# Kernel optimization log

Hardware: AMD Instinct MI355X
Metric: run time of the kernel (lower is better)

The kernel has to match this reference:

```python
import jax, jax.numpy as jnp
import numpy as np
from jax import lax

B, CODELEN, COMLEN, NAST, SUBG = 32, 50, 30, 300, 4
EMB, H, ASTHOPS = 300, 256, 2
AST_VOCAB, COM_VOCAB = 10000, 10000


def gru(x, h0, wih, whh, bih, bhh):
    # PyTorch GRU cell semantics. x: [N, T, D], h0: [N, H] -> (ys [N,T,H], hT [N,H])
    xg = jnp.einsum('ntd,gd->ntg', x, wih) + bih  # precompute input gates [N,T,3H]
    def step(h, xt):
        hg = h @ whh.T + bhh
        xr, xz, xn = jnp.split(xt, 3, axis=-1)
        hr, hz, hn = jnp.split(hg, 3, axis=-1)
        r = jax.nn.sigmoid(xr + hr)
        z = jax.nn.sigmoid(xz + hz)
        n = jnp.tanh(xn + r * hn)
        hnew = (1.0 - z) * n + z * h
        return hnew, hnew
    hT, ys = lax.scan(step, h0, jnp.swapaxes(xg, 0, 1))
    return jnp.swapaxes(ys, 0, 1), hT


def dot_attn(q, k):
    # DotProductAttention in eval mode (dropout = identity)
    scale = 1.0 / jnp.sqrt(jnp.asarray(q.shape[-1], q.dtype))
    s = jnp.einsum('bqd,bkd->bqk', q, k) * scale
    return jnp.einsum('bqk,bkd->bqd', jax.nn.softmax(s, axis=-1), k)


def setup_inputs() -> dict:
    key = jax.random.key(0)
    ks = jax.random.split(key, 32)
    def rn(k, shp, sc=0.05):
        return jax.random.normal(k, shp, jnp.float32) * sc
    inp = {}
    inp['x0'] = jax.random.randint(ks[0], (B, CODELEN), 0, AST_VOCAB)
    inp['x1'] = jax.random.randint(ks[1], (B, COMLEN), 0, COM_VOCAB)
    inp['x2'] = jax.random.randint(ks[2], (B, SUBG, NAST), 0, AST_VOCAB)
    inp['adj'] = jax.random.uniform(ks[3], (B, SUBG, NAST, NAST), jnp.float32) * (1.0 / NAST)
    inp['emb_ast'] = rn(ks[4], (AST_VOCAB, EMB), 0.5)
    inp['emb_com'] = rn(ks[5], (COM_VOCAB, EMB), 0.5)
    inp['gru1_wih'] = rn(ks[6], (3 * H, EMB)); inp['gru1_whh'] = rn(ks[7], (3 * H, H))
    inp['gru1_bih'] = rn(ks[8], (3 * H,));    inp['gru1_bhh'] = rn(ks[9], (3 * H,))
    inp['gru2_wih'] = rn(ks[10], (3 * H, EMB)); inp['gru2_whh'] = rn(ks[11], (3 * H, H))
    inp['gru2_bih'] = rn(ks[12], (3 * H,));     inp['gru2_bhh'] = rn(ks[13], (3 * H,))
    inp['gru4_wih'] = rn(ks[14], (3 * H, NAST * EMB), 0.01)
    inp['gru4_whh'] = rn(ks[15], (3 * H, H))
    inp['gru4_bih'] = rn(ks[16], (3 * H,)); inp['gru4_bhh'] = rn(ks[17], (3 * H,))
    inp['gru58_wih'] = rn(ks[18], (SUBG, 3 * H, EMB)); inp['gru58_whh'] = rn(ks[19], (SUBG, 3 * H, H))
    inp['gru58_bih'] = rn(ks[20], (SUBG, 3 * H));      inp['gru58_bhh'] = rn(ks[21], (SUBG, 3 * H))
    inp['gcn_w'] = rn(ks[22], (EMB, EMB)); inp['gcn_b'] = rn(ks[23], (EMB,))
    inp['dense_w'] = rn(ks[24], (H, 3 * H)); inp['dense_b'] = rn(ks[25], (H,))
    inp['lin_w'] = rn(ks[26], (COM_VOCAB, COMLEN * H), 0.01); inp['lin_b'] = rn(ks[27], (COM_VOCAB,))
    return inp


def reference(x0, x1, x2, adj, emb_ast, emb_com,
              gru1_wih, gru1_whh, gru1_bih, gru1_bhh,
              gru2_wih, gru2_whh, gru2_bih, gru2_bhh,
              gru4_wih, gru4_whh, gru4_bih, gru4_bhh,
              gru58_wih, gru58_whh, gru58_bih, gru58_bhh,
              gcn_w, gcn_b, dense_w, dense_b, lin_w, lin_b):
    b = x0.shape[0]
    scale = 1.0 / jnp.sqrt(jnp.float32(H))
    # token encoder + comment decoder
    tencout, tstate = gru(emb_ast[x0], jnp.zeros((b, H), jnp.float32),
                          gru1_wih, gru1_whh, gru1_bih, gru1_bhh)
    decout, _ = gru(emb_com[x1], tstate, gru2_wih, gru2_whh, gru2_bih, gru2_bhh)
    tcontext = dot_attn(decout, tencout)
    # GCN over 4 sub-graphs (torch code mutates astwork in place -> tmp alias sees post-GCN feats)
    astwork = jnp.transpose(emb_ast[x2], (1, 0, 2, 3))  # [4,B,N,300]
    adjp = jnp.transpose(adj, (1, 0, 2, 3))             # [4,B,N,N]
    for _ in range(ASTHOPS):
        support = jnp.einsum('sbnd,de->sbne', astwork, gcn_w)
        astwork = jax.nn.relu(jnp.einsum('sbnm,sbme->sbne', adjp, support) + gcn_b)
    # TimeDistributed(gru4): batch = 4 sub-graphs, sequence = B, input = flattened node feats
    g4in = astwork.reshape(SUBG, b, NAST * EMB)
    g4out, _ = gru(g4in, jnp.zeros((SUBG, H), jnp.float32),
                   gru4_wih, gru4_whh, gru4_bih, gru4_bhh)
    astw = jnp.transpose(g4out, (1, 0, 2))  # [B,4,H]
    ahier = jax.nn.softmax(jnp.einsum('bqd,bsd->bqs', decout, astw) * scale, axis=-1)
    ahier_p = jnp.transpose(ahier, (2, 0, 1))  # [4,B,Q]
    # per-sub-graph node GRUs (gru5..gru8) vmapped over the sub-graph axis
    outs, _ = jax.vmap(gru, in_axes=(0, None, 0, 0, 0, 0))(
        astwork, tstate, gru58_wih, gru58_whh, gru58_bih, gru58_bhh)  # [4,B,N,H]
    sc = jax.nn.softmax(jnp.einsum('bqd,sbkd->sbqk', decout, outs) * scale, axis=-1)
    new_atten = sc * ahier_p[:, :, :, None]  # element_wise_mul with hierarchy weights
    acontext = jnp.einsum('sbqk,sbkd->bqd', new_atten, outs)  # bmm then sum over sub-graphs
    acontext = dot_attn(decout, acontext)
    context = jnp.concatenate([tcontext, decout, acontext], axis=-1)  # [B,Q,768]
    out = jax.nn.relu(context @ dense_w.T + dense_b)
    out = out.reshape(b, -1)  # [B, 7680]
    return out @ lin_w.T + lin_b  # [B, comvocab]
```

## Files before the change

### kernel.cpp

```cpp
#include <hip/hip_runtime.h>
#include <hip/hip_fp16.h>
#include <hip/hip_bf16.h>


typedef __attribute__((ext_vector_type(8))) short  bf16x8;
typedef __attribute__((ext_vector_type(4))) float  f32x4;

__device__ inline unsigned short f2bs(float f) {
  __hip_bfloat16 h = __float2bfloat16(f);
  unsigned short u; __builtin_memcpy(&u, &h, 2); return u;
}
__device__ inline float bs2f(unsigned short u) {
  unsigned v = (unsigned)u << 16;
  float f; __builtin_memcpy(&f, &v, 4); return f;
}
__device__ inline float sigf(float x) { return 1.f / (1.f + __expf(-x)); }
__device__ inline float tanhf_(float x) {
  const float e = __expf(-2.f * fabsf(x));
  return copysignf((1.f - e) / (1.f + e), x);
}

template <bool ABF, bool BBF, int OUTM, bool RELU, bool GATHER = false, bool BKN = false>
__global__ __launch_bounds__(256) void k_mfma(
    const void* __restrict__ Av, long lda, long a_ss, long a_sb,
    const void* __restrict__ Bv, long ldb, long b_ss, long b_sb,
    void* __restrict__ Cv, long ldc, long c_ss, long c_sb,
    const float* __restrict__ bias, long bias_ss,
    const int* __restrict__ gidx,
    int M, int N, int K, int zb, int ksplit)
{
  __shared__ unsigned short As[128][40];
  __shared__ unsigned short Bs[128][40];
  const int tid = threadIdx.x;
  const int zi = blockIdx.z;
  const int bi = zi / ksplit;
  const int ks = zi - bi * ksplit;
  const int sIdx = bi / zb;
  const int bIdx = bi - sIdx * zb;
  const int row0 = blockIdx.y * 128;
  const int col0 = blockIdx.x * 128;
  const int Kc = ((K + ksplit * 32 - 1) / (ksplit * 32)) * 32;
  const int kbeg = ks * Kc;
  const int kend = min(K, kbeg + Kc);
  if (kbeg >= kend) return;

  const char* Ab = (const char*)Av + ((long)sIdx * a_ss + (long)bIdx * a_sb) * (ABF ? 2 : 4);
  const char* Bb = (const char*)Bv + ((long)sIdx * b_ss + (long)bIdx * b_sb) * (BBF ? 2 : 4);
  char* Cb = (char*)Cv + ((long)sIdx * c_ss + (long)bIdx * c_sb) * ((OUTM == 1 || OUTM == 3) ? 2 : 4);

  const int w = tid >> 6, l = tid & 63;
  const int wr = w >> 1, wc = w & 1;
  const int lr = l & 15, lg = l >> 4;

  f32x4 acc[4][4];
#pragma unroll
  for (int m = 0; m < 4; ++m)
#pragma unroll
    for (int n = 0; n < 4; ++n) acc[m][n] = f32x4{0.f, 0.f, 0.f, 0.f};

  const int sr = tid >> 1;
  const int sk = (tid & 1) * 16;

  for (int kt = kbeg; kt < kend; kt += 32) {
    {
      const int gr = row0 + sr;
      if (ABF) {
        const unsigned short* src = (const unsigned short*)(Ab + ((long)gr * lda + kt + sk) * 2);
        if (gr < M && kt + sk + 16 <= kend) {
          const uint2* p = (const uint2*)src;
          *(uint2*)&As[sr][sk + 0]  = p[0];
          *(uint2*)&As[sr][sk + 4]  = p[1];
          *(uint2*)&As[sr][sk + 8]  = p[2];
          *(uint2*)&As[sr][sk + 12] = p[3];
        } else {
#pragma unroll
          for (int i = 0; i < 16; ++i) {
            const int kk = kt + sk + i;
            As[sr][sk + i] = (gr < M && kk < kend) ? src[i] : (unsigned short)0;
          }
        }
      } else {
        const float* src;
        if (GATHER) src = (const float*)Av + ((gr < M) ? (long)gidx[gr] * lda : 0) + kt + sk;
        else        src = (const float*)(Ab + ((long)gr * lda + kt + sk) * 4);
        if (gr < M && kt + sk + 16 <= kend) {
#pragma unroll
          for (int q = 0; q < 4; ++q) {
            const float4 v = ((const float4*)src)[q];
            *(unsigned*)&As[sr][sk + q * 4 + 0] = (unsigned)f2bs(v.x) | ((unsigned)f2bs(v.y) << 16);
            *(unsigned*)&As[sr][sk + q * 4 + 2] = (unsigned)f2bs(v.z) | ((unsigned)f2bs(v.w) << 16);
          }
        } else {
#pragma unroll
          for (int i = 0; i < 16; ++i) {
            const int kk = kt + sk + i;
            As[sr][sk + i] = (gr < M && kk < kend) ? f2bs(src[i]) : (unsigned short)0;
          }
        }
      }
    }
    if (BKN) {
      const int kk = tid >> 3;
      const int cb = (tid & 7) * 16;
      const int gk = kt + kk;
#pragma unroll
      for (int q = 0; q < 16; ++q) {
        const int gc = col0 + cb + q;
        unsigned short v = 0;
        if (gk < kend && gc < N) {
          if (BBF) v = ((const unsigned short*)Bb)[(long)gk * ldb + gc];
          else     v = f2bs(((const float*)Bb)[(long)gk * ldb + gc]);
        }
        Bs[cb + q][kk] = v;
      }
    } else {
      const int gc = col0 + sr;
      if (BBF) {
        const unsigned short* src = (const unsigned short*)(Bb + ((long)gc * ldb + kt + sk) * 2);
        if (gc < N && kt + sk + 16 <= kend) {
          const uint2* p = (const uint2*)src;
          *(uint2*)&Bs[sr][sk + 0]  = p[0];
          *(uint2*)&Bs[sr][sk + 4]  = p[1];
          *(uint2*)&Bs[sr][sk + 8]  = p[2];
          *(uint2*)&Bs[sr][sk + 12] = p[3];
        } else {
#pragma unroll
          for (int i = 0; i < 16; ++i) {
            const int kk = kt + sk + i;
            Bs[sr][sk + i] = (gc < N && kk < kend) ? src[i] : (unsigned short)0;
          }
        }
      } else {
        const float* src = (const float*)(Bb + ((long)gc * ldb + kt + sk) * 4);
        if (gc < N && kt + sk + 16 <= kend) {
#pragma unroll
          for (int q = 0; q < 4; ++q) {
            const float4 v = ((const float4*)src)[q];
            *(unsigned*)&Bs[sr][sk + q * 4 + 0] = (unsigned)f2bs(v.x) | ((unsigned)f2bs(v.y) << 16);
            *(unsigned*)&Bs[sr][sk + q * 4 + 2] = (unsigned)f2bs(v.z) | ((unsigned)f2bs(v.w) << 16);
          }
        } else {
#pragma unroll
          for (int i = 0; i < 16; ++i) {
            const int kk = kt + sk + i;
            Bs[sr][sk + i] = (gc < N && kk < kend) ? f2bs(src[i]) : (unsigned short)0;
          }
        }
      }
    }
    __syncthreads();
    bf16x8 af[4], bf[4];
#pragma unroll
    for (int m = 0; m < 4; ++m)
      af[m] = *(const bf16x8*)&As[wr * 64 + m * 16 + lr][lg * 8];
#pragma unroll
    for (int n = 0; n < 4; ++n)
      bf[n] = *(const bf16x8*)&Bs[wc * 64 + n * 16 + lr][lg * 8];
#pragma unroll
    for (int m = 0; m < 4; ++m)
#pragma unroll
      for (int n = 0; n < 4; ++n)
        acc[m][n] = __builtin_amdgcn_mfma_f32_16x16x32_bf16(af[m], bf[n], acc[m][n], 0, 0, 0);
    __syncthreads();
  }

  const float* bp = bias ? bias + (long)sIdx * bias_ss : nullptr;
#pragma unroll
  for (int m = 0; m < 4; ++m) {
#pragma unroll
    for (int n = 0; n < 4; ++n) {
      const int col = col0 + wc * 64 + n * 16 + lr;
      const int rb  = row0 + wr * 64 + m * 16 + lg * 4;
      const f32x4 v = acc[m][n];
      if (col >= N) continue;
      if (OUTM == 3) {
        unsigned short* ct = (unsigned short*)Cb + (long)col * ldc + rb;
        if (rb + 4 <= M) {
          ushort4 pk;
          pk.x = f2bs(v[0]); pk.y = f2bs(v[1]); pk.z = f2bs(v[2]); pk.w = f2bs(v[3]);
          *(ushort4*)ct = pk;
        } else {
#pragma unroll
          for (int r = 0; r < 4; ++r) if (rb + r < M) ct[r] = f2bs(v[r]);
        }
      } else {
        const float bv = bp ? bp[col] : 0.f;
#pragma unroll
        for (int r = 0; r < 4; ++r) {
          const int row = rb + r;
          if (row >= M) continue;
          float x = v[r] + bv;
          if (RELU) x = fmaxf(x, 0.f);
          if (OUTM == 0) ((float*)Cb)[(long)row * ldc + col] = x;
          else if (OUTM == 1) ((unsigned short*)Cb)[(long)row * ldc + col] = f2bs(x);
          else atomicAdd((float*)Cb + (long)row * ldc + col, x);
        }
      }
    }
  }
}

template <int CPB, bool XBF, bool YBF>
__global__ __launch_bounds__(512, 2)
void k_gru_v5(
    const void* __restrict__ xg,
    const float* __restrict__ h0, int h0_mod,
    const unsigned short* __restrict__ whh_bf, long w_stride, int cpw,
    const float* __restrict__ bhh, long b_stride,
    void* __restrict__ ys, float* __restrict__ hT, int T)
{
  constexpr int ESZ  = XBF ? 2 : 4;
  constexpr int VPR  = 768 * ESZ / 16;
  constexpr int XVEC = CPB * VPR;
  constexpr int NQ   = (XVEC + 511) / 512;

  const int tid = threadIdx.x;
  const int c0  = blockIdx.x * CPB;
  const int wv  = tid >> 6;
  const int l   = tid & 63;
  const int lr  = l & 15;
  const int lg  = l >> 4;

  __shared__ unsigned short A_lds[2][8][64][8];
  __shared__ unsigned short w_lds[8][8][64][8];
  __shared__ float gate_lds[CPB][772];
  __shared__ float bhh_lds[768];
  __shared__ uint4 xbuf[2][XVEC];

  { unsigned* az = (unsigned*)A_lds;
    for (int i = tid; i < 4096; i += 512) az[i] = 0; }

  const unsigned short* W = whh_bf + (long)(c0 / cpw) * w_stride;
  bf16x8 bfr[5][8];
#pragma unroll
  for (int nt = 0; nt < 5; ++nt) {
    const unsigned short* wp = W + (long)(wv * 96 + nt * 16 + lr) * 256 + lg * 8;
#pragma unroll
    for (int kt = 0; kt < 8; ++kt) bfr[nt][kt] = *(const bf16x8*)(wp + kt * 32);
  }
  {
    const unsigned short* wp = W + (long)(wv * 96 + 5 * 16 + lr) * 256 + lg * 8;
#pragma unroll
    for (int kt = 0; kt < 8; ++kt)
      *(bf16x8*)&w_lds[wv][kt][l][0] = *(const bf16x8*)(wp + kt * 32);
  }
  for (int i = tid; i < 768; i += 512)
    bhh_lds[i] = bhh[(long)(c0 / cpw) * b_stride + i];
  __syncthreads();

  const int c   = tid >> 5;
  const int jb  = tid & 31;
  const bool act = c < CPB;
  const int u0  = jb * 8;

  float h[8];
  if (act) {
#pragma unroll
    for (int e = 0; e < 8; ++e)
      h[e] = h0 ? h0[(long)((c0 + c) % h0_mod) * 256 + u0 + e] : 0.f;
    bf16x8 pk;
#pragma unroll
    for (int e = 0; e < 8; ++e) pk[e] = (short)f2bs(h[e]);
    *(bf16x8*)&A_lds[0][jb >> 2][(jb & 3) * 16 + c][0] = pk;
  }

  const char* xbase = (const char*)xg + (long)c0 * T * 768 * ESZ;
  int poff[NQ]; bool pact[NQ];
#pragma unroll
  for (int q = 0; q < NQ; ++q) {
    const int i = tid + q * 512;
    pact[q] = i < XVEC;
    const int ci = pact[q] ? i / VPR : 0;
    const int of = i - ci * VPR;
    poff[q] = ci * T * 768 * ESZ + of * 16;
  }
#pragma unroll
  for (int q = 0; q < NQ; ++q)
    if (pact[q]) ((uint4*)xbuf[0])[tid + q * 512] = *(const uint4*)(xbase + poff[q]);
  __syncthreads();

  int cur = 0;
  for (int t = 0; t < T; ++t) {
    uint4 xs[NQ];
    const bool pf = (t + 1 < T);
    if (pf) {
#pragma unroll
      for (int q = 0; q < NQ; ++q)
        if (pact[q]) xs[q] = *(const uint4*)(xbase + poff[q] + (long)(t + 1) * 768 * ESZ);
    }

    f32x4 acc[6];
#pragma unroll
    for (int nt = 0; nt < 6; ++nt) acc[nt] = f32x4{0.f, 0.f, 0.f, 0.f};
#pragma unroll
    for (int kt = 0; kt < 8; ++kt) {
      const bf16x8 af = *(const bf16x8*)&A_lds[cur][kt][l][0];
#pragma unroll
      for (int nt = 0; nt < 5; ++nt)
        acc[nt] = __builtin_amdgcn_mfma_f32_16x16x32_bf16(af, bfr[nt][kt], acc[nt], 0, 0, 0);
      const bf16x8 wf = *(const bf16x8*)&w_lds[wv][kt][l][0];
      acc[5] = __builtin_amdgcn_mfma_f32_16x16x32_bf16(af, wf, acc[5], 0, 0, 0);
    }
    if (lg * 4 < CPB) {
#pragma unroll
      for (int nt = 0; nt < 6; ++nt) {
        const int col = wv * 96 + nt * 16 + lr;
#pragma unroll
        for (int r = 0; r < 4; ++r) gate_lds[lg * 4 + r][col] = acc[nt][r];
      }
    }
    __syncthreads();

    if (pf) {
#pragma unroll
      for (int q = 0; q < NQ; ++q)
        if (pact[q]) ((uint4*)xbuf[cur ^ 1])[tid + q * 512] = xs[q];
    }

    if (act) {
      float xr[8], xz[8], xn[8];
      if (XBF) {
        const unsigned short* xp = (const unsigned short*)xbuf[cur] + c * 768;
        const bf16x8 vr = *(const bf16x8*)(xp + u0);
        const bf16x8 vz = *(const bf16x8*)(xp + 256 + u0);
        const bf16x8 vn = *(const bf16x8*)(xp + 512 + u0);
#pragma unroll
        for (int e = 0; e < 8; ++e) {
          xr[e] = bs2f((unsigned short)vr[e]);
          xz[e] = bs2f((unsigned short)vz[e]);
          xn[e] = bs2f((unsigned short)vn[e]);
        }
      } else {
        const float* xp = (const float*)xbuf[cur] + c * 768;
        *(float4*)&xr[0] = *(const float4*)(xp + u0);
        *(float4*)&xr[4] = *(const float4*)(xp + u0 + 4);
        *(float4*)&xz[0] = *(const float4*)(xp + 256 + u0);
        *(float4*)&xz[4] = *(const float4*)(xp + 256 + u0 + 4);
        *(float4*)&xn[0] = *(const float4*)(xp + 512 + u0);
        *(float4*)&xn[4] = *(const float4*)(xp + 512 + u0 + 4);
      }
      bf16x8 pk;
#pragma unroll
      for (int e = 0; e < 8; ++e) {
        const int u = u0 + e;
        const float rr = sigf(xr[e] + gate_lds[c][u] + bhh_lds[u]);
        const float zz = sigf(xz[e] + gate_lds[c][256 + u] + bhh_lds[256 + u]);
        const float nv = tanhf_(xn[e] + rr * (gate_lds[c][512 + u] + bhh_lds[512 + u]));
        h[e] = (1.f - zz) * nv + zz * h[e];
        pk[e] = (short)f2bs(h[e]);
      }
      *(bf16x8*)&A_lds[cur ^ 1][jb >> 2][(jb & 3) * 16 + c][0] = pk;
      if (ys) {
        if (YBF) {
          *(bf16x8*)((unsigned short*)ys + ((long)(c0 + c) * T + t) * 256 + u0) = pk;
        } else {
          float* yp = (float*)ys + ((long)(c0 + c) * T + t) * 256 + u0;
          *(float4*)yp = float4{h[0], h[1], h[2], h[3]};
          *(float4*)(yp + 4) = float4{h[4], h[5], h[6], h[7]};
        }
      }
    }
    __syncthreads();
    cur ^= 1;
  }
  if (hT && act) {
    float* hp = hT + (long)(c0 + c) * 256 + u0;
    *(float4*)hp = float4{h[0], h[1], h[2], h[3]};
    *(float4*)(hp + 4) = float4{h[4], h[5], h[6], h[7]};
  }
}

__global__ __launch_bounds__(256) void k_init_bias(
    float* __restrict__ C, const float* __restrict__ bias, int M, int N)
{
  const int total = M * N;
  for (int i = blockIdx.x * 256 + threadIdx.x; i < total; i += gridDim.x * 256)
    C[i] = bias[i % N];
}

__global__ __launch_bounds__(256) void k_gather_ast(
    const float* __restrict__ emb, const int* __restrict__ x2,
    unsigned short* __restrict__ outp)
{
  const int total = 4 * 32 * 300 * 300;
  for (int idx = blockIdx.x * 256 + threadIdx.x; idx < total; idx += gridDim.x * 256) {
    const int d = idx % 300;
    const int r = idx / 300;
    const int n = r % 300;
    const int r2 = r / 300;
    const int b = r2 % 32;
    const int s = r2 / 32;
    outp[idx] = f2bs(emb[(long)x2[(b * 4 + s) * 300 + n] * 300 + d]);
  }
}

__global__ __launch_bounds__(256) void k_twb(
    const float* __restrict__ w, unsigned short* __restrict__ o, int R, int C)
{
  const int total = R * C;
  for (int i = blockIdx.x * 256 + threadIdx.x; i < total; i += gridDim.x * 256) {
    const int r = i / C, c = i - r * C;
    o[(long)c * R + r] = f2bs(w[i]);
  }
}

__global__ __launch_bounds__(256) void k_f2b(
    const float* __restrict__ a, unsigned short* __restrict__ o, int n)
{
  for (int i = blockIdx.x * 256 + threadIdx.x; i < n; i += gridDim.x * 256)
    o[i] = f2bs(a[i]);
}

__global__ __launch_bounds__(256) void k_attn(
    const float* __restrict__ q, const float* __restrict__ kv,
    float* __restrict__ out, int Q, int L)
{
  const int bq = blockIdx.x;
  const int b = bq / Q;
  const int tid = threadIdx.x;
  const int g = tid >> 3, l = tid & 7;
  __shared__ float qv[256];
  __shared__ float sc[64];
  qv[tid] = q[(long)bq * 256 + tid];
  __syncthreads();
  for (int k0 = 0; k0 < L; k0 += 32) {
    const int k = k0 + g;
    float s = 0.f;
    if (k < L) {
      const float* kr = kv + ((long)b * L + k) * 256;
      for (int d = l; d < 256; d += 8) s += qv[d] * kr[d];
    }
    s += __shfl_xor(s, 1);
    s += __shfl_xor(s, 2);
    s += __shfl_xor(s, 4);
    if (k < L && l == 0) sc[k] = s * 0.0625f;
  }
  __syncthreads();
  float m = -1e30f;
  for (int k = 0; k < L; ++k) m = fmaxf(m, sc[k]);
  float den = 0.f;
  for (int k = 0; k < L; ++k) den += __expf(sc[k] - m);
  __syncthreads();
  if (tid < L) sc[tid] = __expf(sc[tid] - m);
  __syncthreads();
  const float* kb = kv + (long)b * L * 256;
  float acc = 0.f;
  for (int k = 0; k < L; ++k) acc += sc[k] * kb[(long)k * 256 + tid];
  out[(long)bq * 256 + tid] = acc / den;
}

__global__ __launch_bounds__(64) void k_hier(
    const float* __restrict__ dec, const float* __restrict__ g4out,
    float* __restrict__ ahier, int Q)
{
  const int bq = blockIdx.x;
  const int b = bq / Q;
  const int l = threadIdx.x;
  float s[4] = {0.f, 0.f, 0.f, 0.f};
#pragma unroll
  for (int i = 0; i < 4; ++i) {
    const int d = l * 4 + i;
    const float qd = dec[(long)bq * 256 + d];
#pragma unroll
    for (int sg = 0; sg < 4; ++sg)
      s[sg] += qd * g4out[((long)sg * 32 + b) * 256 + d];
  }
#pragma unroll
  for (int off = 32; off >= 1; off >>= 1)
#pragma unroll
    for (int sg = 0; sg < 4; ++sg) s[sg] += __shfl_xor(s[sg], off);
  if (l == 0) {
    float m = -1e30f;
#pragma unroll
    for (int sg = 0; sg < 4; ++sg) m = fmaxf(m, s[sg] * 0.0625f);
    float e[4], den = 0.f;
#pragma unroll
    for (int sg = 0; sg < 4; ++sg) { e[sg] = __expf(s[sg] * 0.0625f - m); den += e[sg]; }
#pragma unroll
    for (int sg = 0; sg < 4; ++sg) ahier[(long)bq * 4 + sg] = e[sg] / den;
  }
}

__global__ __launch_bounds__(64) void k_smax(
    float* __restrict__ sc, const float* __restrict__ ahier)
{
  const int id = blockIdx.x;
  const int s = id / 960;
  const int bq = id - s * 960;
  float* row = sc + (long)id * 300;
  const int l = threadIdx.x;
  float v[5];
  float m = -1e30f;
#pragma unroll
  for (int i = 0; i < 5; ++i) {
    const int k = l + i * 64;
    v[i] = (k < 300) ? row[k] * 0.0625f : -1e30f;
    m = fmaxf(m, v[i]);
  }
#pragma unroll
  for (int off = 32; off >= 1; off >>= 1) m = fmaxf(m, __shfl_xor(m, off));
  float den = 0.f;
#pragma unroll
  for (int i = 0; i < 5; ++i) { v[i] = __expf(v[i] - m); den += v[i]; }
#pragma unroll
  for (int off = 32; off >= 1; off >>= 1) den += __shfl_xor(den, off);
  const float w = ahier[(long)bq * 4 + s] / den;
#pragma unroll
  for (int i = 0; i < 5; ++i) {
    const int k = l + i * 64;
    if (k < 300) row[k] = v[i] * w;
  }
}

__global__ __launch_bounds__(256) void k_concat(
    const float* __restrict__ a, const float* __restrict__ b,
    const float* __restrict__ c, float* __restrict__ out, int rows)
{
  const int total = rows * 768;
  for (int i = blockIdx.x * 256 + threadIdx.x; i < total; i += gridDim.x * 256) {
    const int r = i / 768, col = i - r * 768;
    float v;
    if (col < 256) v = a[(long)r * 256 + col];
    else if (col < 512) v = b[(long)r * 256 + col - 256];
    else v = c[(long)r * 256 + col - 512];
    out[i] = v;
  }
}

extern "C" void kernel_launch(void* const* d_in, const int* in_sizes, int n_in,
                              void* d_out, int out_size, void* d_ws, size_t ws_size,
                              hipStream_t stream) {
  const int*   x0      = (const int*)d_in[0];
  const int*   x1      = (const int*)d_in[1];
  const int*   x2      = (const int*)d_in[2];
  const float* adj     = (const float*)d_in[3];
  const float* emb_ast = (const float*)d_in[4];
  const float* emb_com = (const float*)d_in[5];
  const float* g1_wih  = (const float*)d_in[6];
  const float* g1_whh  = (const float*)d_in[7];
  const float* g1_bih  = (const float*)d_in[8];
  const float* g1_bhh  = (const float*)d_in[9];
  const float* g2_wih  = (const float*)d_in[10];
  const float* g2_whh  = (const float*)d_in[11];
  const float* g2_bih  = (const float*)d_in[12];
  const float* g2_bhh  = (const float*)d_in[13];
  const float* g4_wih  = (const float*)d_in[14];
  const float* g4_whh  = (const float*)d_in[15];
  const float* g4_bih  = (const float*)d_in[16];
  const float* g4_bhh  = (const float*)d_in[17];
  const float* g58_wih = (const float*)d_in[18];
  const float* g58_whh = (const float*)d_in[19];
  const float* g58_bih = (const float*)d_in[20];
  const float* g58_bhh = (const float*)d_in[21];
  const float* gcn_w   = (const float*)d_in[22];
  const float* gcn_b   = (const float*)d_in[23];
  const float* dw      = (const float*)d_in[24];
  const float* db      = (const float*)d_in[25];
  const float* lw      = (const float*)d_in[26];
  const float* lb      = (const float*)d_in[27];
  float* out = (float*)d_out;
  float* ws  = (float*)d_ws;

  unsigned short* astwork_bf = (unsigned short*)ws;
  unsigned short* supportT   = (unsigned short*)(ws + 5760000L);
  unsigned short* g58xg_bf   = (unsigned short*)(ws + 11520000L);
  unsigned short* outsb_bf   = (unsigned short*)(ws + 26265600L);
  unsigned short* xg1_bf     = (unsigned short*)(ws + 31180800L);
  unsigned short* xg2_bf     = (unsigned short*)(ws + 31795200L);
  float* tenc    = ws + 32163840L;
  float* tstate  = ws + 32573440L;
  float* dec     = ws + 32581632L;
  float* tctx    = ws + 32827392L;
  float* g4xg    = ws + 33073152L;
  float* g4out   = ws + 33171456L;
  float* ahier   = ws + 33204224L;
  float* actx1   = ws + 33208064L;
  float* actx    = ws + 33453824L;
  float* dense   = ws + 33699584L;
  float* ctmp    = ws + 33945344L;
  float* scbuf   = ws + 34682624L;
  unsigned short* gcn_wT    = (unsigned short*)(ws + 35834624L);
  unsigned short* dense_bf  = (unsigned short*)(ws + 35879624L);
  unsigned short* g1whh_bf  = (unsigned short*)(ws + 36002504L);
  unsigned short* g2whh_bf  = (unsigned short*)(ws + 36100808L);
  unsigned short* g4whh_bf  = (unsigned short*)(ws + 36199112L);
  unsigned short* g58whh_bf = (unsigned short*)(ws + 36297416L);
  unsigned short* adj_bf    = (unsigned short*)(ws + 36690632L);

  const dim3 blk(256);

  k_gather_ast<<<dim3(4096), blk, 0, stream>>>(emb_ast, x2, astwork_bf);
  k_twb<<<dim3(90), blk, 0, stream>>>(gcn_w, gcn_wT, 300, 300);
  k_f2b<<<dim3(192), blk, 0, stream>>>(g1_whh, g1whh_bf, 196608);
  k_f2b<<<dim3(192), blk, 0, stream>>>(g2_whh, g2whh_bf, 196608);
  k_f2b<<<dim3(192), blk, 0, stream>>>(g4_whh, g4whh_bf, 196608);
  k_f2b<<<dim3(768), blk, 0, stream>>>(g58_whh, g58whh_bf, 786432);
  k_f2b<<<dim3(4096), blk, 0, stream>>>(adj, adj_bf, 11520000);

  for (int hop = 0; hop < 2; ++hop) {
    k_mfma<true, true, 3, false><<<dim3(3, 3, 128), blk, 0, stream>>>(
        astwork_bf, 300, 2880000, 90000,
        gcn_wT, 300, 0, 0,
        supportT, 300, 2880000, 90000,
        nullptr, 0, nullptr, 300, 300, 300, 32, 1);
    k_mfma<true, true, 1, true><<<dim3(3, 3, 128), blk, 0, stream>>>(
        adj_bf, 300, 90000, 360000,
        supportT, 300, 2880000, 90000,
        astwork_bf, 300, 2880000, 90000,
        gcn_b, 0, nullptr, 300, 300, 300, 32, 1);
  }

  k_mfma<false, false, 1, false, true><<<dim3(6, 13, 1), blk, 0, stream>>>(
      emb_ast, 300, 0, 0, g1_wih, 300, 0, 0, xg1_bf, 768, 0, 0,
      g1_bih, 0, x0, 1600, 768, 300, 1, 1);
  k_gru_v5<8, true, false><<<dim3(4), dim3(512), 0, stream>>>(
      xg1_bf, nullptr, 1, g1whh_bf, 0, 32, g1_bhh, 0, tenc, tstate, 50);

  k_mfma<false, false, 1, false, true><<<dim3(6, 8, 1), blk, 0, stream>>>(
      emb_com, 300, 0, 0, g2_wih, 300, 0, 0, xg2_bf, 768, 0, 0,
      g2_bih, 0, x1, 960, 768, 300, 1, 1);
  k_gru_v5<8, true, false><<<dim3(4), dim3(512), 0, stream>>>(
      xg2_bf, tstate, 32, g2whh_bf, 0, 32, g2_bhh, 0, dec, nullptr, 30);

  k_attn<<<dim3(960), blk, 0, stream>>>(dec, tenc, tctx, 30, 50);

  k_init_bias<<<dim3(384), blk, 0, stream>>>(g4xg, g4_bih, 128, 768);
  k_mfma<true, false, 2, false><<<dim3(6, 1, 43), blk, 0, stream>>>(
      astwork_bf, 90000, 0, 0, g4_wih, 90000, 0, 0, g4xg, 768, 0, 0,
      nullptr, 0, nullptr, 128, 768, 90000, 1, 43);
  k_gru_v5<4, false, false><<<dim3(1), dim3(512), 0, stream>>>(
      g4xg, nullptr, 1, g4whh_bf, 0, 4, g4_bhh, 0, g4out, nullptr, 32);

  k_hier<<<dim3(960), dim3(64), 0, stream>>>(dec, g4out, ahier, 30);

  k_mfma<true, false, 1, false><<<dim3(6, 75, 4), blk, 0, stream>>>(
      astwork_bf, 300, 2880000, 0, g58_wih, 300, 230400, 0,
      g58xg_bf, 768, 7372800, 0, g58_bih, 768, nullptr, 9600, 768, 300, 1, 1);
  k_gru_v5<8, true, true><<<dim3(16), dim3(512), 0, stream>>>(
      g58xg_bf, tstate, 32, g58whh_bf, 196608, 32, g58_bhh, 768,
      outsb_bf, nullptr, 300);

  k_mfma<false, true, 0, false><<<dim3(3, 1, 128), blk, 0, stream>>>(
      dec, 256, 0, 7680, outsb_bf, 256, 2457600, 76800, scbuf, 300, 288000, 9000,
      nullptr, 0, nullptr, 30, 300, 256, 32, 1);
  k_smax<<<dim3(3840), dim3(64), 0, stream>>>(scbuf, ahier);
  hipMemsetAsync(actx1, 0, 245760 * sizeof(float), stream);
  k_mfma<false, true, 2, false, false, true><<<dim3(2, 1, 128), blk, 0, stream>>>(
      scbuf, 300, 288000, 9000, outsb_bf, 256, 2457600, 76800, actx1, 256, 0, 7680,
      nullptr, 0, nullptr, 30, 256, 300, 32, 1);

  k_attn<<<dim3(960), blk, 0, stream>>>(dec, actx1, actx, 30, 30);

  k_concat<<<dim3(2880), blk, 0, stream>>>(tctx, dec, actx, ctmp, 960);
  k_mfma<false, false, 0, true><<<dim3(2, 8, 1), blk, 0, stream>>>(
      ctmp, 768, 0, 0, dw, 768, 0, 0, dense, 256, 0, 0,
      db, 0, nullptr, 960, 256, 768, 1, 1);
  k_f2b<<<dim3(960), blk, 0, stream>>>(dense, dense_bf, 245760);

  k_init_bias<<<dim3(1250), blk, 0, stream>>>(out, lb, 32, 10000);
  k_mfma<true, false, 2, false><<<dim3(79, 1, 6), blk, 0, stream>>>(
      dense_bf, 7680, 0, 0, lw, 7680, 0, 0, out, 10000, 0, 0,
      nullptr, 0, nullptr, 32, 10000, 7680, 1, 6);
}
```

Before: 2.012 ms.

## Remap GRU thread layout to drop A double buffer and x LDS staging

Replaces the GRU recurrence kernel with a version where each thread owns hidden units matching the MFMA A-fragment layout, so the hidden state is written in place to a single LDS buffer instead of a double buffer. Input gates are prefetched straight from global memory into registers instead of being staged through LDS. The generic __syncthreads calls become raw s_barrier with explicit lgkmcnt waits and scheduling fences. The g4 input gates are now converted to bf16 by an extra kernel so every call uses bf16 inputs. This is meant to cut per-step LDS traffic and barrier overhead on the serial critical path, at the cost of lower precision for g4 and reliance on hand-placed barrier semantics.

```diff
diff --git a/kernel.cpp b/kernel.cpp
--- a/kernel.cpp
+++ b/kernel.cpp
@@ -200,20 +200,15 @@
   }
 }
 
-template <int CPB, bool XBF, bool YBF>
+template <int CPB, bool YBF>
 __global__ __launch_bounds__(512, 2)
-void k_gru_v5(
-    const void* __restrict__ xg,
+void k_gru_v6(
+    const unsigned short* __restrict__ xg,
     const float* __restrict__ h0, int h0_mod,
     const unsigned short* __restrict__ whh_bf, long w_stride, int cpw,
     const float* __restrict__ bhh, long b_stride,
     void* __restrict__ ys, float* __restrict__ hT, int T)
 {
-  constexpr int ESZ  = XBF ? 2 : 4;
-  constexpr int VPR  = 768 * ESZ / 16;
-  constexpr int XVEC = CPB * VPR;
-  constexpr int NQ   = (XVEC + 511) / 512;
-
   const int tid = threadIdx.x;
   const int c0  = blockIdx.x * CPB;
   const int wv  = tid >> 6;
@@ -221,14 +216,10 @@
   const int lr  = l & 15;
   const int lg  = l >> 4;
 
-  __shared__ unsigned short A_lds[2][8][64][8];
+  __shared__ unsigned short A_lds[512][8];
   __shared__ unsigned short w_lds[8][8][64][8];
   __shared__ float gate_lds[CPB][772];
   __shared__ float bhh_lds[768];
-  __shared__ uint4 xbuf[2][XVEC];
-
-  { unsigned* az = (unsigned*)A_lds;
-    for (int i = tid; i < 4096; i += 512) az[i] = 0; }
 
   const unsigned short* W = whh_bf + (long)(c0 / cpw) * w_stride;
   bf16x8 bfr[5][8];
@@ -239,62 +230,47 @@
     for (int kt = 0; kt < 8; ++kt) bfr[nt][kt] = *(const bf16x8*)(wp + kt * 32);
   }
   {
-    const unsigned short* wp = W + (long)(wv * 96 + 5 * 16 + lr) * 256 + lg * 8;
+    const unsigned short* wp = W + (long)(wv * 96 + 80 + lr) * 256 + lg * 8;
 #pragma unroll
     for (int kt = 0; kt < 8; ++kt)
       *(bf16x8*)&w_lds[wv][kt][l][0] = *(const bf16x8*)(wp + kt * 32);
   }
   for (int i = tid; i < 768; i += 512)
     bhh_lds[i] = bhh[(long)(c0 / cpw) * b_stride + i];
+
+  const bool act = lr < CPB;
+  const int cO  = lr;
+  const int u0  = wv * 32 + lg * 8;
+
+  float h[8];
+  {
+    bf16x8 pk;
+#pragma unroll
+    for (int e = 0; e < 8; ++e) {
+      float hv = 0.f;
+      if (act && h0) hv = h0[(long)((c0 + cO) % h0_mod) * 256 + u0 + e];
+      h[e] = hv;
+      pk[e] = (short)f2bs(hv);
+    }
+    *(bf16x8*)&A_lds[tid][0] = pk;
+  }
+
+  const unsigned short* xrow = xg + (long)(c0 + cO) * T * 768 + u0;
+  bf16x8 xv0, xv1, xv2;
+  if (act) {
+    xv0 = *(const bf16x8*)(xrow);
+    xv1 = *(const bf16x8*)(xrow + 256);
+    xv2 = *(const bf16x8*)(xrow + 512);
+  }
   __syncthreads();
 
-  const int c   = tid >> 5;
-  const int jb  = tid & 31;
-  const bool act = c < CPB;
-  const int u0  = jb * 8;
-
-  float h[8];
-  if (act) {
-#pragma unroll
-    for (int e = 0; e < 8; ++e)
-      h[e] = h0 ? h0[(long)((c0 + c) % h0_mod) * 256 + u0 + e] : 0.f;
-    bf16x8 pk;
-#pragma unroll
-    for (int e = 0; e < 8; ++e) pk[e] = (short)f2bs(h[e]);
-    *(bf16x8*)&A_lds[0][jb >> 2][(jb & 3) * 16 + c][0] = pk;
-  }
-
-  const char* xbase = (const char*)xg + (long)c0 * T * 768 * ESZ;
-  int poff[NQ]; bool pact[NQ];
-#pragma unroll
-  for (int q = 0; q < NQ; ++q) {
-    const int i = tid + q * 512;
-    pact[q] = i < XVEC;
-    const int ci = pact[q] ? i / VPR : 0;
-    const int of = i - ci * VPR;
-    poff[q] = ci * T * 768 * ESZ + of * 16;
-  }
-#pragma unroll
-  for (int q = 0; q < NQ; ++q)
-    if (pact[q]) ((uint4*)xbuf[0])[tid + q * 512] = *(const uint4*)(xbase + poff[q]);
-  __syncthreads();
-
-  int cur = 0;
   for (int t = 0; t < T; ++t) {
-    uint4 xs[NQ];
-    const bool pf = (t + 1 < T);
-    if (pf) {
-#pragma unroll
-      for (int q = 0; q < NQ; ++q)
-        if (pact[q]) xs[q] = *(const uint4*)(xbase + poff[q] + (long)(t + 1) * 768 * ESZ);
-    }
-
     f32x4 acc[6];
 #pragma unroll
     for (int nt = 0; nt < 6; ++nt) acc[nt] = f32x4{0.f, 0.f, 0.f, 0.f};
 #pragma unroll
     for (int kt = 0; kt < 8; ++kt) {
-      const bf16x8 af = *(const bf16x8*)&A_lds[cur][kt][l][0];
+      const bf16x8 af = *(const bf16x8*)&A_lds[kt * 64 + l][0];
 #pragma unroll
       for (int nt = 0; nt < 5; ++nt)
         acc[nt] = __builtin_amdgcn_mfma_f32_16x16x32_bf16(af, bfr[nt][kt], acc[nt], 0, 0, 0);
@@ -309,62 +285,51 @@
         for (int r = 0; r < 4; ++r) gate_lds[lg * 4 + r][col] = acc[nt][r];
       }
     }
-    __syncthreads();
-
-    if (pf) {
-#pragma unroll
-      for (int q = 0; q < NQ; ++q)
-        if (pact[q]) ((uint4*)xbuf[cur ^ 1])[tid + q * 512] = xs[q];
-    }
+    asm volatile("s_waitcnt lgkmcnt(0)" ::: "memory");
+    __builtin_amdgcn_sched_barrier(0);
+    __builtin_amdgcn_s_barrier();
+    __builtin_amdgcn_sched_barrier(0);
 
     if (act) {
       float xr[8], xz[8], xn[8];
-      if (XBF) {
-        const unsigned short* xp = (const unsigned short*)xbuf[cur] + c * 768;
-        const bf16x8 vr = *(const bf16x8*)(xp + u0);
-        const bf16x8 vz = *(const bf16x8*)(xp + 256 + u0);
-        const bf16x8 vn = *(const bf16x8*)(xp + 512 + u0);
-#pragma unroll
-        for (int e = 0; e < 8; ++e) {
-          xr[e] = bs2f((unsigned short)vr[e]);
-          xz[e] = bs2f((unsigned short)vz[e]);
-          xn[e] = bs2f((unsigned short)vn[e]);
-        }
-      } else {
-        const float* xp = (const float*)xbuf[cur] + c * 768;
-        *(float4*)&xr[0] = *(const float4*)(xp + u0);
-        *(float4*)&xr[4] = *(const float4*)(xp + u0 + 4);
-        *(float4*)&xz[0] = *(const float4*)(xp + 256 + u0);
-        *(float4*)&xz[4] = *(const float4*)(xp + 256 + u0 + 4);
-        *(float4*)&xn[0] = *(const float4*)(xp + 512 + u0);
-        *(float4*)&xn[4] = *(const float4*)(xp + 512 + u0 + 4);
+#pragma unroll
+      for (int e = 0; e < 8; ++e) {
+        xr[e] = bs2f((unsigned short)xv0[e]);
+        xz[e] = bs2f((unsigned short)xv1[e]);
+        xn[e] = bs2f((unsigned short)xv2[e]);
       }
       bf16x8 pk;
 #pragma unroll
       for (int e = 0; e < 8; ++e) {
         const int u = u0 + e;
-        const float rr = sigf(xr[e] + gate_lds[c][u] + bhh_lds[u]);
-        const float zz = sigf(xz[e] + gate_lds[c][256 + u] + bhh_lds[256 + u]);
-        const float nv = tanhf_(xn[e] + rr * (gate_lds[c][512 + u] + bhh_lds[512 + u]));
+        const float rr = sigf(xr[e] + gate_lds[cO][u] + bhh_lds[u]);
+        const float zz = sigf(xz[e] + gate_lds[cO][256 + u] + bhh_lds[256 + u]);
+        const float nv = tanhf_(xn[e] + rr * (gate_lds[cO][512 + u] + bhh_lds[512 + u]));
         h[e] = (1.f - zz) * nv + zz * h[e];
         pk[e] = (short)f2bs(h[e]);
       }
-      *(bf16x8*)&A_lds[cur ^ 1][jb >> 2][(jb & 3) * 16 + c][0] = pk;
-      if (ys) {
-        if (YBF) {
-          *(bf16x8*)((unsigned short*)ys + ((long)(c0 + c) * T + t) * 256 + u0) = pk;
-        } else {
-          float* yp = (float*)ys + ((long)(c0 + c) * T + t) * 256 + u0;
-          *(float4*)yp = float4{h[0], h[1], h[2], h[3]};
-          *(float4*)(yp + 4) = float4{h[4], h[5], h[6], h[7]};
-        }
-      }
-    }
-    __syncthreads();
-    cur ^= 1;
-  }
-  if (hT && act) {
-    float* hp = hT + (long)(c0 + c) * 256 + u0;
+      *(bf16x8*)&A_lds[tid][0] = pk;
+      if (YBF) {
+        *(bf16x8*)((unsigned short*)ys + ((long)(c0 + cO) * T + t) * 256 + u0) = pk;
+      } else {
+        float* yp = (float*)ys + ((long)(c0 + cO) * T + t) * 256 + u0;
+        *(float4*)yp = float4{h[0], h[1], h[2], h[3]};
+        *(float4*)(yp + 4) = float4{h[4], h[5], h[6], h[7]};
+      }
+      if (t + 1 < T) {
+        const unsigned short* xp = xrow + (long)(t + 1) * 768;
+        xv0 = *(const bf16x8*)(xp);
+        xv1 = *(const bf16x8*)(xp + 256);
+        xv2 = *(const bf16x8*)(xp + 512);
+      }
+    }
+    asm volatile("s_waitcnt lgkmcnt(0)" ::: "memory");
+    __builtin_amdgcn_sched_barrier(0);
+    __builtin_amdgcn_s_barrier();
+    __builtin_amdgcn_sched_barrier(0);
+  }
+  if (act && hT) {
+    float* hp = hT + (long)(c0 + cO) * 256 + u0;
     *(float4*)hp = float4{h[0], h[1], h[2], h[3]};
     *(float4*)(hp + 4) = float4{h[4], h[5], h[6], h[7]};
   }
@@ -586,6 +551,7 @@
   unsigned short* g4whh_bf  = (unsigned short*)(ws + 36199112L);
   unsigned short* g58whh_bf = (unsigned short*)(ws + 36297416L);
   unsigned short* adj_bf    = (unsigned short*)(ws + 36690632L);
+  unsigned short* g4xg_bf   = (unsigned short*)(ws + 42450632L);
 
   const dim3 blk(256);
 
@@ -613,13 +579,13 @@
   k_mfma<false, false, 1, false, true><<<dim3(6, 13, 1), blk, 0, stream>>>(
       emb_ast, 300, 0, 0, g1_wih, 300, 0, 0, xg1_bf, 768, 0, 0,
       g1_bih, 0, x0, 1600, 768, 300, 1, 1);
-  k_gru_v5<8, true, false><<<dim3(4), dim3(512), 0, stream>>>(
+  k_gru_v6<8, false><<<dim3(4), dim3(512), 0, stream>>>(
       xg1_bf, nullptr, 1, g1whh_bf, 0, 32, g1_bhh, 0, tenc, tstate, 50);
 
   k_mfma<false, false, 1, false, true><<<dim3(6, 8, 1), blk, 0, stream>>>(
       emb_com, 300, 0, 0, g2_wih, 300, 0, 0, xg2_bf, 768, 0, 0,
       g2_bih, 0, x1, 960, 768, 300, 1, 1);
-  k_gru_v5<8, true, false><<<dim3(4), dim3(512), 0, stream>>>(
+  k_gru_v6<8, false><<<dim3(4), dim3(512), 0, stream>>>(
       xg2_bf, tstate, 32, g2whh_bf, 0, 32, g2_bhh, 0, dec, nullptr, 30);
 
   k_attn<<<dim3(960), blk, 0, stream>>>(dec, tenc, tctx, 30, 50);
@@ -628,15 +594,16 @@
   k_mfma<true, false, 2, false><<<dim3(6, 1, 43), blk, 0, stream>>>(
       astwork_bf, 90000, 0, 0, g4_wih, 90000, 0, 0, g4xg, 768, 0, 0,
       nullptr, 0, nullptr, 128, 768, 90000, 1, 43);
-  k_gru_v5<4, false, false><<<dim3(1), dim3(512), 0, stream>>>(
-      g4xg, nullptr, 1, g4whh_bf, 0, 4, g4_bhh, 0, g4out, nullptr, 32);
+  k_f2b<<<dim3(384), blk, 0, stream>>>(g4xg, g4xg_bf, 98304);
+  k_gru_v6<4, false><<<dim3(1), dim3(512), 0, stream>>>(
+      g4xg_bf, nullptr, 1, g4whh_bf, 0, 4, g4_bhh, 0, g4out, nullptr, 32);
 
   k_hier<<<dim3(960), dim3(64), 0, stream>>>(dec, g4out, ahier, 30);
 
   k_mfma<true, false, 1, false><<<dim3(6, 75, 4), blk, 0, stream>>>(
       astwork_bf, 300, 2880000, 0, g58_wih, 300, 230400, 0,
       g58xg_bf, 768, 7372800, 0, g58_bih, 768, nullptr, 9600, 768, 300, 1, 1);
-  k_gru_v5<8, true, true><<<dim3(16), dim3(512), 0, stream>>>(
+  k_gru_v6<8, true><<<dim3(16), dim3(512), 0, stream>>>(
       g58xg_bf, tstate, 32, g58whh_bf, 196608, 32, g58_bhh, 768,
       outsb_bf, nullptr, 300);
 
```

Result: slower. 2.104 ms (+4.6%).
